# Kernel optimization log

Measured on AMD Instinct MI355X. Metric: run time of the kernel, lower is better.

The kernel has to match this reference:

```python
import jax, jax.numpy as jnp
import numpy as np

THRESH = 0.5
MARGIN = 0.1
SCALE_POS = 2.0
SCALE_NEG = 40.0
EPS = 1e-5


def setup_inputs() -> dict:
    key = jax.random.key(0)
    k1, k2 = jax.random.split(key)
    B, D, C = 8192, 512, 512
    feats = jax.random.normal(k1, (B, D), dtype=jnp.float32)
    labels = jax.random.randint(k2, (B,), 0, C, dtype=jnp.int32)
    return {"feats": feats, "labels": labels}


def reference(feats, labels):
    B = feats.shape[0]
    inv_b = 1.0 / B
    # L2-normalize rows, cosine similarity matrix [B, B]
    f = feats / jnp.linalg.norm(feats, axis=1, keepdims=True)
    sim = f @ f.T

    same = labels[:, None] == labels[None, :]
    # positive pairs: same label AND sim < 1 - eps (excludes self-similarity)
    pos_mask = same & (sim < 1.0 - EPS)
    neg_mask = ~same

    pos_cnt = jnp.sum(pos_mask, axis=1)
    neg_cnt = jnp.sum(neg_mask, axis=1)
    valid1 = (pos_cnt >= 1) & (neg_cnt >= 1)  # row contributes to avg_ap/avg_an

    pos_sum_sim = jnp.sum(jnp.where(pos_mask, sim, 0.0), axis=1)
    neg_sum_sim = jnp.sum(jnp.where(neg_mask, sim, 0.0), axis=1)
    mean_pos = pos_sum_sim / jnp.maximum(pos_cnt, 1)
    mean_neg = neg_sum_sim / jnp.maximum(neg_cnt, 1)

    min_pos = jnp.min(jnp.where(pos_mask, sim, jnp.inf), axis=1)
    max_neg = jnp.max(jnp.where(neg_mask, sim, -jnp.inf), axis=1)

    # hard mining: neg_pair + margin > min(pos), pos_pair - margin < max(neg)
    neg_sel = neg_mask & (sim + MARGIN > min_pos[:, None])
    pos_sel = pos_mask & (sim - MARGIN < max_neg[:, None])
    valid2 = (jnp.sum(pos_sel, axis=1) >= 1) & (jnp.sum(neg_sel, axis=1) >= 1)
    valid = valid1 & valid2

    pos_exp = jnp.sum(jnp.where(pos_sel, jnp.exp(-SCALE_POS * (sim - THRESH)), 0.0), axis=1)
    neg_exp = jnp.sum(jnp.where(neg_sel, jnp.exp(SCALE_NEG * (sim - THRESH)), 0.0), axis=1)
    row_loss = (1.0 / SCALE_POS) * jnp.log1p(pos_exp) + (1.0 / SCALE_NEG) * jnp.log1p(neg_exp)

    loss = jnp.sum(jnp.where(valid, row_loss, 0.0)) * inv_b
    avg_ap = jnp.sum(jnp.where(valid1, mean_pos, 0.0)) * inv_b
    avg_an = jnp.sum(jnp.where(valid1, mean_neg, 0.0)) * inv_b
    return (loss.reshape(-1), avg_ap, avg_an)
```

## Files before the change

kernel.cpp:

```cpp
#include <hip/hip_runtime.h>
#include <math.h>

typedef float floatx4 __attribute__((ext_vector_type(4)));
typedef short short8 __attribute__((ext_vector_type(8)));
typedef unsigned short ushort4v __attribute__((ext_vector_type(4)));
typedef unsigned short ushort8v __attribute__((ext_vector_type(8)));

#define MARGIN_ 0.1f
#define THRESH_ 0.5f

__device__ __forceinline__ unsigned short f2bf(float f){
  unsigned int x = __float_as_uint(f);
  x += 0x7FFFu + ((x >> 16) & 1u);
  return (unsigned short)(x >> 16);
}
__device__ __forceinline__ float bf2f(unsigned short u){
  return __uint_as_float(((unsigned int)u) << 16);
}

__device__ __forceinline__ void gld16(const unsigned short* g, unsigned short* l){
  __builtin_amdgcn_global_load_lds(
      (const __attribute__((address_space(1))) unsigned int*)(g),
      (__attribute__((address_space(3))) unsigned int*)(l), 16, 0, 0);
}

__global__ __launch_bounds__(64) void k_norm(const float* __restrict__ feats,
                                             unsigned short* __restrict__ fbf){
  const int row = blockIdx.x;
  const int l = threadIdx.x;
  const float* rp = feats + (size_t)row * 512;
  float4 v0 = ((const float4*)rp)[2 * l];
  float4 v1 = ((const float4*)rp)[2 * l + 1];
  float ss = v0.x*v0.x + v0.y*v0.y + v0.z*v0.z + v0.w*v0.w
           + v1.x*v1.x + v1.y*v1.y + v1.z*v1.z + v1.w*v1.w;
  #pragma unroll
  for(int m = 1; m < 64; m <<= 1) ss += __shfl_xor(ss, m);
  const float rn = 1.0f / sqrtf(ss);
  short8 pk;
  pk[0] = (short)f2bf(v0.x*rn); pk[1] = (short)f2bf(v0.y*rn);
  pk[2] = (short)f2bf(v0.z*rn); pk[3] = (short)f2bf(v0.w*rn);
  pk[4] = (short)f2bf(v1.x*rn); pk[5] = (short)f2bf(v1.y*rn);
  pk[6] = (short)f2bf(v1.z*rn); pk[7] = (short)f2bf(v1.w*rn);
  ((short8*)(fbf + (size_t)row * 512))[l] = pk;
}

__global__ __launch_bounds__(256) void k_prep(const int* __restrict__ labels,
                                              unsigned short* __restrict__ labp,
                                              int* __restrict__ cnt, int Bn){
  const int i = blockIdx.x * 256 + threadIdx.x;
  if(i < Bn){
    labp[i] = (unsigned short)labels[(i & ~63) + ((i & 3) * 16) + ((i >> 2) & 15)];
    atomicAdd(&cnt[labels[i]], 1);
  }
}

#define TRI_S(y) ((y)*n - (((y)*((y)-1))>>1))
__global__ __launch_bounds__(256) void k_gemm_sym(const unsigned short* __restrict__ fbf,
                                                  unsigned short* __restrict__ simb,
                                                  int Bn, int nTri){
  const int n = Bn >> 7;
  int i = blockIdx.x;
  int j;
  if((nTri & 7) == 0){ const int c = nTri >> 3; j = (i & 7) * c + (i >> 3); }
  else j = i;
  int by = (int)(((float)(2*n + 1) - sqrtf((float)((2*n+1)*(2*n+1) - 8*j))) * 0.5f);
  if(by < 0) by = 0;
  while(TRI_S(by + 1) <= j) by++;
  while(TRI_S(by) > j) by--;
  const int bx = by + (j - TRI_S(by));
  const bool diag = (by == bx);

  __shared__ __align__(16) unsigned short Ald[128 * 32];
  __shared__ __align__(16) unsigned short Bld[128 * 32];

  const int t = threadIdx.x;
  const int lane = t & 63, wave = t >> 6;
  const int wm = wave >> 1, wn = wave & 1;
  const int lc = lane & 15, lk = lane >> 4;
  const int row0 = by * 128, col0 = bx * 128;

  floatx4 acc[4][4];
  #pragma unroll
  for(int a = 0; a < 4; a++)
    #pragma unroll
    for(int b2 = 0; b2 < 4; b2++) acc[a][b2] = (floatx4){0.f, 0.f, 0.f, 0.f};

  const int rsub  = lane >> 2;
  const int slotg = (lane & 3) ^ ((lane >> 3) & 3);
  const unsigned short* gA0 = fbf + (size_t)(row0 + wave*32 + rsub) * 512 + slotg * 8;
  const unsigned short* gB0 = fbf + (size_t)(col0 + wave*32 + rsub) * 512 + slotg * 8;
  unsigned short* lA0 = Ald + wave * 1024;
  unsigned short* lB0 = Bld + wave * 1024;
  const int kswz = lk ^ ((lc >> 1) & 3);

  for(int k0 = 0; k0 < 512; k0 += 32){
    __syncthreads();
    gld16(gA0 + k0,            lA0);
    gld16(gA0 + 16*512 + k0,   lA0 + 512);
    gld16(gB0 + k0,            lB0);
    gld16(gB0 + 16*512 + k0,   lB0 + 512);
    __syncthreads();
    short8 av[4], bv[4];
    #pragma unroll
    for(int mi = 0; mi < 4; mi++) av[mi] = ((const short8*)Ald)[(wm*64 + mi*16 + lc)*4 + kswz];
    #pragma unroll
    for(int ni = 0; ni < 4; ni++) bv[ni] = ((const short8*)Bld)[(wn*64 + ni*16 + lc)*4 + kswz];
    #pragma unroll
    for(int mi = 0; mi < 4; mi++)
      #pragma unroll
      for(int ni = 0; ni < 4; ni++)
        acc[mi][ni] = __builtin_amdgcn_mfma_f32_16x16x32_bf16(av[mi], bv[ni], acc[mi][ni], 0, 0, 0);
  }

  unsigned short b[4][4][4];
  #pragma unroll
  for(int mi = 0; mi < 4; mi++)
    #pragma unroll
    for(int ni = 0; ni < 4; ni++)
      #pragma unroll
      for(int r = 0; r < 4; r++) b[mi][ni][r] = f2bf(acc[mi][ni][r]);

  #pragma unroll
  for(int mi = 0; mi < 4; mi++){
    #pragma unroll
    for(int r = 0; r < 4; r++){
      const int row = row0 + wm*64 + mi*16 + lk*4 + r;
      ushort4v v;
      v[0] = b[mi][0][r]; v[1] = b[mi][1][r]; v[2] = b[mi][2][r]; v[3] = b[mi][3][r];
      *(ushort4v*)(simb + (size_t)row * Bn + col0 + wn*64 + lc*4) = v;
    }
  }

  if(!diag){
    #pragma unroll
    for(int ni = 0; ni < 4; ni++){
      const size_t crow = (size_t)(col0 + wn*64 + ni*16 + lc) * Bn;
      #pragma unroll
      for(int h = 0; h < 2; h++){
        ushort8v v;
        v[0] = b[0][ni][2*h];   v[1] = b[1][ni][2*h];
        v[2] = b[2][ni][2*h];   v[3] = b[3][ni][2*h];
        v[4] = b[0][ni][2*h+1]; v[5] = b[1][ni][2*h+1];
        v[6] = b[2][ni][2*h+1]; v[7] = b[3][ni][2*h+1];
        *(ushort8v*)(simb + crow + row0 + wm*64 + 16*lk + 8*h) = v;
      }
    }
  }
}

template<int NPT>
__global__ __launch_bounds__(256) void k_fused4(const unsigned short* __restrict__ simb,
                                                const int* __restrict__ labels,
                                                const unsigned short* __restrict__ labp,
                                                const int* __restrict__ cnt,
                                                float* __restrict__ rl,
                                                float* __restrict__ apv,
                                                float* __restrict__ anv, int Bn){
  const int t = threadIdx.x, lane = t & 63, wave = t >> 6;
  __shared__ float rq0[4], rq1[4], rq2[4], rq3[4];
  __shared__ int fl[2];

  for(int rr = 0; rr < 4; rr++){
    const int row = blockIdx.x * 4 + rr;
    __syncthreads();
    if(t < 2) fl[t] = 0;
    __syncthreads();

    const unsigned short* srow = simb + (size_t)row * Bn;
    const int labi = labels[row];
    const int a = row & 63;
    const int selfpos = (row & ~63) + ((a & 15) * 4) + (a >> 4);

    ushort8v sv[NPT];
    unsigned int pmask[NPT], nmask[NPT];

    float ps = 0.f, tot = 0.f, mn = INFINITY, mx = -INFINITY;
    #pragma unroll
    for(int c = 0; c < NPT; c++){
      const int idx = c * 256 + t;
      sv[c] = ((const ushort8v*)srow)[idx];
      const ushort8v lb = ((const ushort8v*)labp)[idx];
      const int j0 = idx * 8;
      const unsigned int selfm =
          ((unsigned int)(selfpos - j0) < 8u) ? (1u << (selfpos - j0)) : 0u;
      unsigned int sm = 0;
      #pragma unroll
      for(int e = 0; e < 8; e++) sm |= (((int)lb[e] == labi) ? 1u : 0u) << e;
      const unsigned int pm = sm & ~selfm;
      pmask[c] = pm;
      nmask[c] = (~sm) & 0xFFu;
      #pragma unroll
      for(int e = 0; e < 8; e++){
        const float s = bf2f(sv[c][e]);
        tot += s;
        const bool p = (pm >> e) & 1u;
        const bool nn = (nmask[c] >> e) & 1u;
        ps += p ? s : 0.f;
        mn = p ? fminf(mn, s) : mn;
        mx = nn ? fmaxf(mx, s) : mx;
      }
      if(selfm) tot -= bf2f(sv[c][selfpos - j0]);
    }
    #pragma unroll
    for(int m = 1; m < 64; m <<= 1){
      ps += __shfl_xor(ps, m); tot += __shfl_xor(tot, m);
      mn = fminf(mn, __shfl_xor(mn, m)); mx = fmaxf(mx, __shfl_xor(mx, m));
    }
    if(lane == 0){ rq0[wave] = ps; rq1[wave] = tot; rq2[wave] = mn; rq3[wave] = mx; }
    __syncthreads();
    const float bps    = rq0[0] + rq0[1] + rq0[2] + rq0[3];
    const float btot   = rq1[0] + rq1[1] + rq1[2] + rq1[3];
    const float minpos = fminf(fminf(rq2[0], rq2[1]), fminf(rq2[2], rq2[3]));
    const float maxneg = fmaxf(fmaxf(rq3[0], rq3[1]), fmaxf(rq3[2], rq3[3]));
    __syncthreads();

    float pe = 0.f, ne = 0.f;
    bool pA = false, nA = false;
    #pragma unroll
    for(int c = 0; c < NPT; c++){
      #pragma unroll
      for(int e = 0; e < 8; e++){
        const float s = bf2f(sv[c][e]);
        const bool psel = ((pmask[c] >> e) & 1u) && (s - MARGIN_ < maxneg);
        const bool nsel = ((nmask[c] >> e) & 1u) && (s + MARGIN_ > minpos);
        const float arg = psel ? (THRESH_ - s) * 2.0f : (s - THRESH_) * 40.0f;
        const float ex = __expf(arg);
        pe += psel ? ex : 0.f;
        ne += nsel ? ex : 0.f;
        pA = pA || psel;
        nA = nA || nsel;
      }
    }
    const unsigned long long bp = __ballot((int)pA);
    const unsigned long long bn = __ballot((int)nA);
    #pragma unroll
    for(int m = 1; m < 64; m <<= 1){
      pe += __shfl_xor(pe, m); ne += __shfl_xor(ne, m);
    }
    if(lane == 0){
      rq0[wave] = pe; rq1[wave] = ne;
      if(bp) fl[0] = 1;
      if(bn) fl[1] = 1;
    }
    __syncthreads();
    if(t == 0){
      const float spe = rq0[0] + rq0[1] + rq0[2] + rq0[3];
      const float sne = rq1[0] + rq1[1] + rq1[2] + rq1[3];
      const int c = cnt[labi];
      const float pc = (float)(c - 1);
      const float nc = (float)(Bn - c);
      const bool v1 = (pc >= 1.f) && (nc >= 1.f);
      const bool valid = v1 && (fl[0] != 0) && (fl[1] != 0);
      rl[row]  = valid ? (0.5f * log1pf(spe) + 0.025f * log1pf(sne)) : 0.f;
      apv[row] = v1 ? bps / fmaxf(pc, 1.f) : 0.f;
      anv[row] = v1 ? (btot - bps) / fmaxf(nc, 1.f) : 0.f;
    }
  }
}

__global__ __launch_bounds__(256) void k_fused_gen(const unsigned short* __restrict__ simb,
                                                   const int* __restrict__ labels,
                                                   const unsigned short* __restrict__ labp,
                                                   const int* __restrict__ cnt,
                                                   float* __restrict__ rl,
                                                   float* __restrict__ apv,
                                                   float* __restrict__ anv, int Bn){
  const int row = blockIdx.x;
  const int t = threadIdx.x, lane = t & 63, wave = t >> 6;
  const unsigned short* srow = simb + (size_t)row * Bn;
  const int labi = labels[row];
  const int a = row & 63;
  const int selfpos = (row & ~63) + ((a & 15) * 4) + (a >> 4);
  const int npt = Bn >> 11;

  __shared__ float rq0[4], rq1[4], rq2[4], rq3[4];
  __shared__ int fl[2];
  if(t < 2) fl[t] = 0;

  float ps = 0.f, tot = 0.f, mn = INFINITY, mx = -INFINITY;
  for(int c2 = 0; c2 < npt; c2++){
    const int idx = c2 * 256 + t;
    const ushort8v svv = ((const ushort8v*)srow)[idx];
    const ushort8v lb = ((const ushort8v*)labp)[idx];
    const int j0 = idx * 8;
    #pragma unroll
    for(int e = 0; e < 8; e++){
      const float s = bf2f(svv[e]);
      const bool same = ((int)lb[e] == labi);
      const bool self = ((j0 + e) == selfpos);
      if(!self) tot += s;
      if(same && !self){ ps += s; mn = fminf(mn, s); }
      if(!same) mx = fmaxf(mx, s);
    }
  }
  #pragma unroll
  for(int m = 1; m < 64; m <<= 1){
    ps += __shfl_xor(ps, m); tot += __shfl_xor(tot, m);
    mn = fminf(mn, __shfl_xor(mn, m)); mx = fmaxf(mx, __shfl_xor(mx, m));
  }
  if(lane == 0){ rq0[wave] = ps; rq1[wave] = tot; rq2[wave] = mn; rq3[wave] = mx; }
  __syncthreads();
  const float bps    = rq0[0] + rq0[1] + rq0[2] + rq0[3];
  const float btot   = rq1[0] + rq1[1] + rq1[2] + rq1[3];
  const float minpos = fminf(fminf(rq2[0], rq2[1]), fminf(rq2[2], rq2[3]));
  const float maxneg = fmaxf(fmaxf(rq3[0], rq3[1]), fmaxf(rq3[2], rq3[3]));
  __syncthreads();

  float pe = 0.f, ne = 0.f;
  bool pA = false, nA = false;
  for(int c2 = 0; c2 < npt; c2++){
    const int idx = c2 * 256 + t;
    const ushort8v svv = ((const ushort8v*)srow)[idx];
    const ushort8v lb = ((const ushort8v*)labp)[idx];
    const int j0 = idx * 8;
    #pragma unroll
    for(int e = 0; e < 8; e++){
      const float s = bf2f(svv[e]);
      const bool same = ((int)lb[e] == labi);
      const bool self = ((j0 + e) == selfpos);
      const bool psel = same && !self && (s - MARGIN_ < maxneg);
      const bool nsel = (!same) && (s + MARGIN_ > minpos);
      const float arg = psel ? (THRESH_ - s) * 2.0f : (s - THRESH_) * 40.0f;
      const float ex = __expf(arg);
      pe += psel ? ex : 0.f;
      ne += nsel ? ex : 0.f;
      pA = pA || psel;
      nA = nA || nsel;
    }
  }
  const unsigned long long bp = __ballot((int)pA);
  const unsigned long long bn = __ballot((int)nA);
  #pragma unroll
  for(int m = 1; m < 64; m <<= 1){
    pe += __shfl_xor(pe, m); ne += __shfl_xor(ne, m);
  }
  if(lane == 0){
    rq0[wave] = pe; rq1[wave] = ne;
    if(bp) fl[0] = 1;
    if(bn) fl[1] = 1;
  }
  __syncthreads();
  if(t == 0){
    const float spe = rq0[0] + rq0[1] + rq0[2] + rq0[3];
    const float sne = rq1[0] + rq1[1] + rq1[2] + rq1[3];
    const int c = cnt[labi];
    const float pc = (float)(c - 1);
    const float nc = (float)(Bn - c);
    const bool v1 = (pc >= 1.f) && (nc >= 1.f);
    const bool valid = v1 && (fl[0] != 0) && (fl[1] != 0);
    rl[row]  = valid ? (0.5f * log1pf(spe) + 0.025f * log1pf(sne)) : 0.f;
    apv[row] = v1 ? bps / fmaxf(pc, 1.f) : 0.f;
    anv[row] = v1 ? (btot - bps) / fmaxf(nc, 1.f) : 0.f;
  }
}

__global__ __launch_bounds__(256) void k_sum(const float* __restrict__ rl,
                                             const float* __restrict__ apv,
                                             const float* __restrict__ anv,
                                             float* __restrict__ blk, int Bn){
  const int t = threadIdx.x;
  const int row = blockIdx.x * 256 + t;
  float r = rl[row], a1 = apv[row], a2 = anv[row];
  #pragma unroll
  for(int off = 32; off; off >>= 1){
    r += __shfl_down(r, off); a1 += __shfl_down(a1, off); a2 += __shfl_down(a2, off);
  }
  __shared__ float red[3][4];
  const int lane = t & 63, wave = t >> 6;
  if(lane == 0){ red[0][wave] = r; red[1][wave] = a1; red[2][wave] = a2; }
  __syncthreads();
  if(t == 0){
    blk[blockIdx.x*3 + 0] = red[0][0] + red[0][1] + red[0][2] + red[0][3];
    blk[blockIdx.x*3 + 1] = red[1][0] + red[1][1] + red[1][2] + red[1][3];
    blk[blockIdx.x*3 + 2] = red[2][0] + red[2][1] + red[2][2] + red[2][3];
  }
}

__global__ void k_final(const float* __restrict__ blk, int nblk, float inv_b,
                        float* __restrict__ out){
  if(threadIdx.x == 0 && blockIdx.x == 0){
    float l = 0, a = 0, n = 0;
    for(int i = 0; i < nblk; i++){ l += blk[i*3]; a += blk[i*3 + 1]; n += blk[i*3 + 2]; }
    out[0] = l * inv_b;
    out[1] = a * inv_b;
    out[2] = n * inv_b;
  }
}

__global__ __launch_bounds__(256) void k_pass1(const unsigned short* __restrict__ fbf,
                                               const int* __restrict__ labels,
                                               float* __restrict__ part,
                                               int Bn, int ncb){
  __shared__ __align__(16) unsigned short Ald[128 * 32];
  __shared__ __align__(16) unsigned short Bld[128 * 32];
  __shared__ int Lrow[128], Lcol[128];
  __shared__ float Sps[2][128], Stot[2][128], Smin[2][128], Smax[2][128];

  const int t = threadIdx.x;
  const int lane = t & 63, wave = t >> 6;
  const int wm = wave >> 1, wn = wave & 1;
  const int lc = lane & 15, lk = lane >> 4;
  const int row0 = blockIdx.y * 128, col0 = blockIdx.x * 128;

  if(t < 128){
    Lrow[t] = labels[row0 + t];
    Lcol[t] = labels[col0 + t];
  }

  floatx4 acc[4][4];
  #pragma unroll
  for(int i = 0; i < 4; i++)
    #pragma unroll
    for(int j = 0; j < 4; j++) acc[i][j] = (floatx4){0.f, 0.f, 0.f, 0.f};

  const int rsub  = lane >> 2;
  const int slotg = (lane & 3) ^ ((lane >> 3) & 3);
  const unsigned short* gA0 = fbf + (size_t)(row0 + wave*32 + rsub) * 512 + slotg * 8;
  const unsigned short* gB0 = fbf + (size_t)(col0 + wave*32 + rsub) * 512 + slotg * 8;
  unsigned short* lA0 = Ald + wave * 1024;
  unsigned short* lB0 = Bld + wave * 1024;
  const int kswz = lk ^ ((lc >> 1) & 3);

  for(int k0 = 0; k0 < 512; k0 += 32){
    __syncthreads();
    gld16(gA0 + k0,            lA0);
    gld16(gA0 + 16*512 + k0,   lA0 + 512);
    gld16(gB0 + k0,            lB0);
    gld16(gB0 + 16*512 + k0,   lB0 + 512);
    __syncthreads();
    short8 av[4], bv[4];
    #pragma unroll
    for(int mi = 0; mi < 4; mi++) av[mi] = ((const short8*)Ald)[(wm*64 + mi*16 + lc)*4 + kswz];
    #pragma unroll
    for(int ni = 0; ni < 4; ni++) bv[ni] = ((const short8*)Bld)[(wn*64 + ni*16 + lc)*4 + kswz];
    #pragma unroll
    for(int mi = 0; mi < 4; mi++)
      #pragma unroll
      for(int ni = 0; ni < 4; ni++)
        acc[mi][ni] = __builtin_amdgcn_mfma_f32_16x16x32_bf16(av[mi], bv[ni], acc[mi][ni], 0, 0, 0);
  }

  int labj[4], gj[4];
  #pragma unroll
  for(int ni = 0; ni < 4; ni++){
    const int cl = wn*64 + ni*16 + lc;
    labj[ni] = Lcol[cl]; gj[ni] = col0 + cl;
  }
  #pragma unroll
  for(int mi = 0; mi < 4; mi++){
    #pragma unroll
    for(int r = 0; r < 4; r++){
      const int rowl = wm*64 + mi*16 + lk*4 + r;
      const int labi = Lrow[rowl];
      const int gi = row0 + rowl;
      float ps = 0.f, tot = 0.f, mn = INFINITY, mx = -INFINITY;
      #pragma unroll
      for(int ni = 0; ni < 4; ni++){
        const float s = acc[mi][ni][r];
        const bool same = (labi == labj[ni]);
        const bool self = (gi == gj[ni]);
        if(!self) tot += s;
        if(same && !self){ ps += s; mn = fminf(mn, s); }
        if(!same) mx = fmaxf(mx, s);
      }
      #pragma unroll
      for(int m = 1; m < 16; m <<= 1){
        ps += __shfl_xor(ps, m); tot += __shfl_xor(tot, m);
        mn = fminf(mn, __shfl_xor(mn, m)); mx = fmaxf(mx, __shfl_xor(mx, m));
      }
      if(lc == 0){
        Sps[wn][rowl] = ps; Stot[wn][rowl] = tot;
        Smin[wn][rowl] = mn; Smax[wn][rowl] = mx;
      }
    }
  }
  __syncthreads();
  if(t < 128){
    const size_t stride = (size_t)ncb * Bn;
    const size_t base = (size_t)blockIdx.x * Bn + row0 + t;
    part[0*stride + base] = Sps[0][t] + Sps[1][t];
    part[1*stride + base] = Stot[0][t] + Stot[1][t];
    part[2*stride + base] = fminf(Smin[0][t], Smin[1][t]);
    part[3*stride + base] = fmaxf(Smax[0][t], Smax[1][t]);
  }
}

__global__ __launch_bounds__(256) void k_reduce1(const float* __restrict__ part,
                                                 const int* __restrict__ labels,
                                                 const int* __restrict__ cnt,
                                                 float* __restrict__ st,
                                                 int Bn, int ncb){
  const int row = blockIdx.x * 256 + threadIdx.x;
  if(row >= Bn) return;
  const size_t stride = (size_t)ncb * Bn;
  float ps = 0, tot = 0, mn = INFINITY, mx = -INFINITY;
  for(int cb = 0; cb < ncb; cb++){
    const size_t base = (size_t)cb * Bn + row;
    ps  += part[0*stride + base];
    tot += part[1*stride + base];
    mn = fminf(mn, part[2*stride + base]);
    mx = fmaxf(mx, part[3*stride + base]);
  }
  const int c = cnt[labels[row]];
  const float pc = (float)(c - 1);
  const float nc = (float)(Bn - c);
  st[0*Bn + row] = mn;
  st[1*Bn + row] = mx;
  st[2*Bn + row] = ps / fmaxf(pc, 1.f);
  st[3*Bn + row] = (tot - ps) / fmaxf(nc, 1.f);
  st[4*Bn + row] = (pc >= 1.f && nc >= 1.f) ? 1.f : 0.f;
}

__global__ __launch_bounds__(256) void k_pass2(const unsigned short* __restrict__ fbf,
                                               const int* __restrict__ labels,
                                               const float* __restrict__ st,
                                               float* __restrict__ part,
                                               int Bn, int ncb){
  __shared__ __align__(16) unsigned short Ald[128 * 32];
  __shared__ __align__(16) unsigned short Bld[128 * 32];
  __shared__ int Lrow[128], Lcol[128];
  __shared__ float Minp[128], Maxn[128];
  __shared__ float Spe[2][128], Sne[2][128], Spf[2][128], Snf[2][128];

  const int t = threadIdx.x;
  const int lane = t & 63, wave = t >> 6;
  const int wm = wave >> 1, wn = wave & 1;
  const int lc = lane & 15, lk = lane >> 4;
  const int row0 = blockIdx.y * 128, col0 = blockIdx.x * 128;

  if(t < 128){
    Lrow[t] = labels[row0 + t];
    Lcol[t] = labels[col0 + t];
    Minp[t] = st[0*Bn + row0 + t];
    Maxn[t] = st[1*Bn + row0 + t];
  }

  floatx4 acc[4][4];
  #pragma unroll
  for(int i = 0; i < 4; i++)
    #pragma unroll
    for(int j = 0; j < 4; j++) acc[i][j] = (floatx4){0.f, 0.f, 0.f, 0.f};

  const int rsub  = lane >> 2;
  const int slotg = (lane & 3) ^ ((lane >> 3) & 3);
  const unsigned short* gA0 = fbf + (size_t)(row0 + wave*32 + rsub) * 512 + slotg * 8;
  const unsigned short* gB0 = fbf + (size_t)(col0 + wave*32 + rsub) * 512 + slotg * 8;
  unsigned short* lA0 = Ald + wave * 1024;
  unsigned short* lB0 = Bld + wave * 1024;
  const int kswz = lk ^ ((lc >> 1) & 3);

  for(int k0 = 0; k0 < 512; k0 += 32){
    __syncthreads();
    gld16(gA0 + k0,            lA0);
    gld16(gA0 + 16*512 + k0,   lA0 + 512);
    gld16(gB0 + k0,            lB0);
    gld16(gB0 + 16*512 + k0,   lB0 + 512);
    __syncthreads();
    short8 av[4], bv[4];
    #pragma unroll
    for(int mi = 0; mi < 4; mi++) av[mi] = ((const short8*)Ald)[(wm*64 + mi*16 + lc)*4 + kswz];
    #pragma unroll
    for(int ni = 0; ni < 4; ni++) bv[ni] = ((const short8*)Bld)[(wn*64 + ni*16 + lc)*4 + kswz];
    #pragma unroll
    for(int mi = 0; mi < 4; mi++)
      #pragma unroll
      for(int ni = 0; ni < 4; ni++)
        acc[mi][ni] = __builtin_amdgcn_mfma_f32_16x16x32_bf16(av[mi], bv[ni], acc[mi][ni], 0, 0, 0);
  }

  int labj[4], gj[4];
  #pragma unroll
  for(int ni = 0; ni < 4; ni++){
    const int cl = wn*64 + ni*16 + lc;
    labj[ni] = Lcol[cl]; gj[ni] = col0 + cl;
  }
  #pragma unroll
  for(int mi = 0; mi < 4; mi++){
    #pragma unroll
    for(int r = 0; r < 4; r++){
      const int rowl = wm*64 + mi*16 + lk*4 + r;
      const int labi = Lrow[rowl];
      const int gi = row0 + rowl;
      const float mp  = Minp[rowl];
      const float mxn = Maxn[rowl];
      float pe = 0.f, ne = 0.f;
      bool pa = false, na = false;
      #pragma unroll
      for(int ni = 0; ni < 4; ni++){
        const float s = acc[mi][ni][r];
        const bool same = (labi == labj[ni]);
        const bool self = (gi == gj[ni]);
        if(same && !self && (s - MARGIN_ < mxn)){
          pe += __expf(-2.0f * (s - THRESH_)); pa = true;
        }
        if(!same && (s + MARGIN_ > mp)){
          ne += __expf(40.0f * (s - THRESH_)); na = true;
        }
      }
      const unsigned long long bp  = __ballot((int)pa);
      const unsigned long long bn2 = __ballot((int)na);
      #pragma unroll
      for(int m = 1; m < 16; m <<= 1){
        pe += __shfl_xor(pe, m); ne += __shfl_xor(ne, m);
      }
      if(lc == 0){
        Spe[wn][rowl] = pe; Sne[wn][rowl] = ne;
        Spf[wn][rowl] = ((bp  >> (lk*16)) & 0xFFFFull) ? 1.f : 0.f;
        Snf[wn][rowl] = ((bn2 >> (lk*16)) & 0xFFFFull) ? 1.f : 0.f;
      }
    }
  }
  __syncthreads();
  if(t < 128){
    const size_t stride = (size_t)ncb * Bn;
    const size_t base = (size_t)blockIdx.x * Bn + row0 + t;
    part[0*stride + base] = Spe[0][t] + Spe[1][t];
    part[1*stride + base] = Sne[0][t] + Sne[1][t];
    part[2*stride + base] = fmaxf(Spf[0][t], Spf[1][t]);
    part[3*stride + base] = fmaxf(Snf[0][t], Snf[1][t]);
  }
}

__global__ __launch_bounds__(256) void k_reduce2f(const float* __restrict__ part,
                                                  const float* __restrict__ st,
                                                  float* __restrict__ rowloss,
                                                  float* __restrict__ apv,
                                                  float* __restrict__ anv,
                                                  int Bn, int ncb){
  const int row = blockIdx.x * 256 + threadIdx.x;
  if(row >= Bn) return;
  const size_t stride = (size_t)ncb * Bn;
  float pe = 0, ne = 0, pf = 0, nf = 0;
  for(int cb = 0; cb < ncb; cb++){
    const size_t base = (size_t)cb * Bn + row;
    pe += part[0*stride + base]; ne += part[1*stride + base];
    pf = fmaxf(pf, part[2*stride + base]); nf = fmaxf(nf, part[3*stride + base]);
  }
  const float v1 = st[4*Bn + row];
  const bool valid = (v1 > 0.5f) && (pf > 0.5f) && (nf > 0.5f);
  rowloss[row] = valid ? (0.5f * log1pf(pe) + 0.025f * log1pf(ne)) : 0.f;
  apv[row] = (v1 > 0.5f) ? st[2*Bn + row] : 0.f;
  anv[row] = (v1 > 0.5f) ? st[3*Bn + row] : 0.f;
}

extern "C" void kernel_launch(void* const* d_in, const int* in_sizes, int n_in,
                              void* d_out, int out_size, void* d_ws, size_t ws_size,
                              hipStream_t stream){
  const float* feats = (const float*)d_in[0];
  const int* labels = (const int*)d_in[1];
  float* out = (float*)d_out;
  const int Bn  = in_sizes[1];
  const int ncb = Bn / 128;
  const int nTri = ncb * (ncb + 1) / 2;

  char* ws = (char*)d_ws;
  size_t off = 0;
  unsigned short* fbf = (unsigned short*)(ws + off); off += (size_t)Bn * 512 * 2;
  float* part = (float*)(ws + off); off += (size_t)4 * ncb * Bn * 4;
  float* st   = (float*)(ws + off); off += (size_t)5 * Bn * 4;
  int*   cnt  = (int*)(ws + off);   off += 4096;
  unsigned short* labp = (unsigned short*)(ws + off); off += (size_t)Bn * 2;
  off = (off + 255) & ~(size_t)255;
  float* rl   = (float*)(ws + off); off += (size_t)Bn * 4;
  float* apv  = (float*)(ws + off); off += (size_t)Bn * 4;
  float* anv  = (float*)(ws + off); off += (size_t)Bn * 4;
  float* blk  = (float*)(ws + off); off += 4096;
  off = (off + 255) & ~(size_t)255;
  unsigned short* simb = (unsigned short*)(ws + off);
  const size_t need = off + (size_t)Bn * Bn * 2;
  const bool mat = (ws_size >= need);

  hipMemsetAsync(cnt, 0, 512 * sizeof(int), stream);
  k_norm<<<Bn, 64, 0, stream>>>(feats, fbf);
  k_prep<<<(Bn + 255) / 256, 256, 0, stream>>>(labels, labp, cnt, Bn);
  if(mat){
    k_gemm_sym<<<nTri, 256, 0, stream>>>(fbf, simb, Bn, nTri);
    if(Bn == 8192){
      k_fused4<4><<<Bn / 4, 256, 0, stream>>>(simb, labels, labp, cnt, rl, apv, anv, Bn);
    } else {
      k_fused_gen<<<Bn, 256, 0, stream>>>(simb, labels, labp, cnt, rl, apv, anv, Bn);
    }
  } else {
    dim3 g(ncb, Bn / 128);
    k_pass1<<<g, 256, 0, stream>>>(fbf, labels, part, Bn, ncb);
    k_reduce1<<<Bn / 256, 256, 0, stream>>>(part, labels, cnt, st, Bn, ncb);
    k_pass2<<<g, 256, 0, stream>>>(fbf, labels, st, part, Bn, ncb);
    k_reduce2f<<<Bn / 256, 256, 0, stream>>>(part, st, rl, apv, anv, Bn, ncb);
  }
  k_sum<<<Bn / 256, 256, 0, stream>>>(rl, apv, anv, blk, Bn);
  k_final<<<1, 64, 0, stream>>>(blk, Bn / 256, 1.0f / (float)Bn, out);
}
```

Before: 161.6 us.

## Use one row per block in fused pass, replace ballot flags with analytic validity

The fused row-reduction kernel now assigns one row per block (grid Bn) instead of looping four rows per block, which removes the per-row barriers and the flag-reset syncs. The any-selected flags are replaced by a closed-form check: a positive is selected iff minpos - margin < maxneg, and a negative iff maxneg + margin > minpos. This drops the ballots and shared flags. The exponent becomes a single exp2f of an fma with log2e-folded constants, and bf16 unpacking works on 32-bit words with shifts and masks. More blocks means more scheduling overhead but more memory-level parallelism. The validity rewrite relies on the min/max equivalence also holding for NaN and infinity edge cases.

```diff
diff --git a/kernel.cpp b/kernel.cpp
--- a/kernel.cpp
+++ b/kernel.cpp
@@ -5,9 +5,11 @@
 typedef short short8 __attribute__((ext_vector_type(8)));
 typedef unsigned short ushort4v __attribute__((ext_vector_type(4)));
 typedef unsigned short ushort8v __attribute__((ext_vector_type(8)));
+typedef unsigned int uint4v __attribute__((ext_vector_type(4)));
 
 #define MARGIN_ 0.1f
 #define THRESH_ 0.5f
+#define LOG2E_ 1.44269504088896f
 
 __device__ __forceinline__ unsigned short f2bf(float f){
   unsigned int x = __float_as_uint(f);
@@ -149,112 +151,116 @@
 }
 
 template<int NPT>
-__global__ __launch_bounds__(256) void k_fused4(const unsigned short* __restrict__ simb,
-                                                const int* __restrict__ labels,
-                                                const unsigned short* __restrict__ labp,
-                                                const int* __restrict__ cnt,
-                                                float* __restrict__ rl,
-                                                float* __restrict__ apv,
-                                                float* __restrict__ anv, int Bn){
+__global__ __launch_bounds__(256) void k_fused(const unsigned short* __restrict__ simb,
+                                               const int* __restrict__ labels,
+                                               const unsigned short* __restrict__ labp,
+                                               const int* __restrict__ cnt,
+                                               float* __restrict__ rl,
+                                               float* __restrict__ apv,
+                                               float* __restrict__ anv, int Bn){
+  const int row = blockIdx.x;
   const int t = threadIdx.x, lane = t & 63, wave = t >> 6;
+  const unsigned short* srow = simb + (size_t)row * Bn;
+  const int labi = labels[row];
+  const int a = row & 63;
+  const int selfpos = (row & ~63) + ((a & 15) * 4) + (a >> 4);
+
   __shared__ float rq0[4], rq1[4], rq2[4], rq3[4];
-  __shared__ int fl[2];
-
-  for(int rr = 0; rr < 4; rr++){
-    const int row = blockIdx.x * 4 + rr;
-    __syncthreads();
-    if(t < 2) fl[t] = 0;
-    __syncthreads();
-
-    const unsigned short* srow = simb + (size_t)row * Bn;
-    const int labi = labels[row];
-    const int a = row & 63;
-    const int selfpos = (row & ~63) + ((a & 15) * 4) + (a >> 4);
-
-    ushort8v sv[NPT];
-    unsigned int pmask[NPT], nmask[NPT];
-
-    float ps = 0.f, tot = 0.f, mn = INFINITY, mx = -INFINITY;
-    #pragma unroll
-    for(int c = 0; c < NPT; c++){
-      const int idx = c * 256 + t;
-      sv[c] = ((const ushort8v*)srow)[idx];
-      const ushort8v lb = ((const ushort8v*)labp)[idx];
-      const int j0 = idx * 8;
-      const unsigned int selfm =
-          ((unsigned int)(selfpos - j0) < 8u) ? (1u << (selfpos - j0)) : 0u;
-      unsigned int sm = 0;
-      #pragma unroll
-      for(int e = 0; e < 8; e++) sm |= (((int)lb[e] == labi) ? 1u : 0u) << e;
-      const unsigned int pm = sm & ~selfm;
-      pmask[c] = pm;
-      nmask[c] = (~sm) & 0xFFu;
-      #pragma unroll
-      for(int e = 0; e < 8; e++){
-        const float s = bf2f(sv[c][e]);
-        tot += s;
-        const bool p = (pm >> e) & 1u;
-        const bool nn = (nmask[c] >> e) & 1u;
-        ps += p ? s : 0.f;
-        mn = p ? fminf(mn, s) : mn;
-        mx = nn ? fmaxf(mx, s) : mx;
-      }
-      if(selfm) tot -= bf2f(sv[c][selfpos - j0]);
-    }
-    #pragma unroll
-    for(int m = 1; m < 64; m <<= 1){
-      ps += __shfl_xor(ps, m); tot += __shfl_xor(tot, m);
-      mn = fminf(mn, __shfl_xor(mn, m)); mx = fmaxf(mx, __shfl_xor(mx, m));
-    }
-    if(lane == 0){ rq0[wave] = ps; rq1[wave] = tot; rq2[wave] = mn; rq3[wave] = mx; }
-    __syncthreads();
-    const float bps    = rq0[0] + rq0[1] + rq0[2] + rq0[3];
-    const float btot   = rq1[0] + rq1[1] + rq1[2] + rq1[3];
-    const float minpos = fminf(fminf(rq2[0], rq2[1]), fminf(rq2[2], rq2[3]));
-    const float maxneg = fmaxf(fmaxf(rq3[0], rq3[1]), fmaxf(rq3[2], rq3[3]));
-    __syncthreads();
-
-    float pe = 0.f, ne = 0.f;
-    bool pA = false, nA = false;
-    #pragma unroll
-    for(int c = 0; c < NPT; c++){
-      #pragma unroll
-      for(int e = 0; e < 8; e++){
-        const float s = bf2f(sv[c][e]);
-        const bool psel = ((pmask[c] >> e) & 1u) && (s - MARGIN_ < maxneg);
-        const bool nsel = ((nmask[c] >> e) & 1u) && (s + MARGIN_ > minpos);
-        const float arg = psel ? (THRESH_ - s) * 2.0f : (s - THRESH_) * 40.0f;
-        const float ex = __expf(arg);
+
+  uint4v sv[NPT];
+  unsigned int pmask[NPT], nmask[NPT];
+
+  float ps = 0.f, tot = 0.f, mn = INFINITY, mx = -INFINITY;
+  #pragma unroll
+  for(int c = 0; c < NPT; c++){
+    const int idx = c * 256 + t;
+    sv[c] = ((const uint4v*)srow)[idx];
+    const uint4v lb = ((const uint4v*)labp)[idx];
+    const int j0 = idx * 8;
+    const int so = selfpos - j0;
+    const unsigned int selfm = ((unsigned int)so < 8u) ? (1u << so) : 0u;
+    unsigned int sm = 0;
+    #pragma unroll
+    for(int k = 0; k < 4; k++){
+      const unsigned int lw = lb[k];
+      sm |= (((int)(lw & 0xFFFFu) == labi) ? 1u : 0u) << (2*k);
+      sm |= (((int)(lw >> 16)     == labi) ? 1u : 0u) << (2*k + 1);
+    }
+    const unsigned int pm = sm & ~selfm;
+    pmask[c] = pm;
+    nmask[c] = (~sm) & 0xFFu;
+    #pragma unroll
+    for(int k = 0; k < 4; k++){
+      const unsigned int w = sv[c][k];
+      const float slo = __uint_as_float(w << 16);
+      const float shi = __uint_as_float(w & 0xFFFF0000u);
+      tot += slo + shi;
+      const bool plo = (pm >> (2*k)) & 1u,  phi = (pm >> (2*k+1)) & 1u;
+      const bool nlo = (nmask[c] >> (2*k)) & 1u, nhi = (nmask[c] >> (2*k+1)) & 1u;
+      ps += plo ? slo : 0.f;  ps += phi ? shi : 0.f;
+      mn = plo ? fminf(mn, slo) : mn;  mn = phi ? fminf(mn, shi) : mn;
+      mx = nlo ? fmaxf(mx, slo) : mx;  mx = nhi ? fmaxf(mx, shi) : mx;
+    }
+    if(selfm){
+      const unsigned int w = sv[c][so >> 1];
+      tot -= (so & 1) ? __uint_as_float(w & 0xFFFF0000u) : __uint_as_float(w << 16);
+    }
+  }
+  #pragma unroll
+  for(int m = 1; m < 64; m <<= 1){
+    ps += __shfl_xor(ps, m); tot += __shfl_xor(tot, m);
+    mn = fminf(mn, __shfl_xor(mn, m)); mx = fmaxf(mx, __shfl_xor(mx, m));
+  }
+  if(lane == 0){ rq0[wave] = ps; rq1[wave] = tot; rq2[wave] = mn; rq3[wave] = mx; }
+  __syncthreads();
+  const float bps    = rq0[0] + rq0[1] + rq0[2] + rq0[3];
+  const float btot   = rq1[0] + rq1[1] + rq1[2] + rq1[3];
+  const float minpos = fminf(fminf(rq2[0], rq2[1]), fminf(rq2[2], rq2[3]));
+  const float maxneg = fmaxf(fmaxf(rq3[0], rq3[1]), fmaxf(rq3[2], rq3[3]));
+
+  const float KP1 = -2.0f * LOG2E_, KP0 = 1.0f * LOG2E_;
+  const float KN1 = 40.0f * LOG2E_, KN0 = -20.0f * LOG2E_;
+  float pe = 0.f, ne = 0.f;
+  #pragma unroll
+  for(int c = 0; c < NPT; c++){
+    const unsigned int pm = pmask[c], nm = nmask[c];
+    #pragma unroll
+    for(int k = 0; k < 4; k++){
+      const unsigned int w = sv[c][k];
+      #pragma unroll
+      for(int h = 0; h < 2; h++){
+        const float s = h ? __uint_as_float(w & 0xFFFF0000u)
+                          : __uint_as_float(w << 16);
+        const int e = 2*k + h;
+        const bool isp = (pm >> e) & 1u;
+        const bool isn = (nm >> e) & 1u;
+        const float ex = exp2f(fmaf(s, isp ? KP1 : KN1, isp ? KP0 : KN0));
+        const bool psel = isp && (s - MARGIN_ < maxneg);
+        const bool nsel = isn && (s + MARGIN_ > minpos);
         pe += psel ? ex : 0.f;
         ne += nsel ? ex : 0.f;
-        pA = pA || psel;
-        nA = nA || nsel;
-      }
-    }
-    const unsigned long long bp = __ballot((int)pA);
-    const unsigned long long bn = __ballot((int)nA);
-    #pragma unroll
-    for(int m = 1; m < 64; m <<= 1){
-      pe += __shfl_xor(pe, m); ne += __shfl_xor(ne, m);
-    }
-    if(lane == 0){
-      rq0[wave] = pe; rq1[wave] = ne;
-      if(bp) fl[0] = 1;
-      if(bn) fl[1] = 1;
-    }
-    __syncthreads();
-    if(t == 0){
-      const float spe = rq0[0] + rq0[1] + rq0[2] + rq0[3];
-      const float sne = rq1[0] + rq1[1] + rq1[2] + rq1[3];
-      const int c = cnt[labi];
-      const float pc = (float)(c - 1);
-      const float nc = (float)(Bn - c);
-      const bool v1 = (pc >= 1.f) && (nc >= 1.f);
-      const bool valid = v1 && (fl[0] != 0) && (fl[1] != 0);
-      rl[row]  = valid ? (0.5f * log1pf(spe) + 0.025f * log1pf(sne)) : 0.f;
-      apv[row] = v1 ? bps / fmaxf(pc, 1.f) : 0.f;
-      anv[row] = v1 ? (btot - bps) / fmaxf(nc, 1.f) : 0.f;
-    }
+      }
+    }
+  }
+  #pragma unroll
+  for(int m = 1; m < 64; m <<= 1){
+    pe += __shfl_xor(pe, m); ne += __shfl_xor(ne, m);
+  }
+  if(lane == 0){ rq0[wave] = pe; rq1[wave] = ne; }
+  __syncthreads();
+  if(t == 0){
+    const float spe = rq0[0] + rq0[1] + rq0[2] + rq0[3];
+    const float sne = rq1[0] + rq1[1] + rq1[2] + rq1[3];
+    const int c = cnt[labi];
+    const float pc = (float)(c - 1);
+    const float nc = (float)(Bn - c);
+    const bool v1 = (pc >= 1.f) && (nc >= 1.f);
+    const bool pf = (minpos - MARGIN_ < maxneg);
+    const bool nf = (maxneg + MARGIN_ > minpos);
+    const bool valid = v1 && pf && nf;
+    rl[row]  = valid ? (0.5f * log1pf(spe) + 0.025f * log1pf(sne)) : 0.f;
+    apv[row] = v1 ? bps / fmaxf(pc, 1.f) : 0.f;
+    anv[row] = v1 ? (btot - bps) / fmaxf(nc, 1.f) : 0.f;
   }
 }
 
@@ -274,8 +280,6 @@
   const int npt = Bn >> 11;
 
   __shared__ float rq0[4], rq1[4], rq2[4], rq3[4];
-  __shared__ int fl[2];
-  if(t < 2) fl[t] = 0;
 
   float ps = 0.f, tot = 0.f, mn = INFINITY, mx = -INFINITY;
   for(int c2 = 0; c2 < npt; c2++){
@@ -304,10 +308,8 @@
   const float btot   = rq1[0] + rq1[1] + rq1[2] + rq1[3];
   const float minpos = fminf(fminf(rq2[0], rq2[1]), fminf(rq2[2], rq2[3]));
   const float maxneg = fmaxf(fmaxf(rq3[0], rq3[1]), fmaxf(rq3[2], rq3[3]));
-  __syncthreads();
 
   float pe = 0.f, ne = 0.f;
-  bool pA = false, nA = false;
   for(int c2 = 0; c2 < npt; c2++){
     const int idx = c2 * 256 + t;
     const ushort8v svv = ((const ushort8v*)srow)[idx];
@@ -320,25 +322,17 @@
       const bool self = ((j0 + e) == selfpos);
       const bool psel = same && !self && (s - MARGIN_ < maxneg);
       const bool nsel = (!same) && (s + MARGIN_ > minpos);
-      const float arg = psel ? (THRESH_ - s) * 2.0f : (s - THRESH_) * 40.0f;
-      const float ex = __expf(arg);
+      const float ex = exp2f(fmaf(s, psel ? (-2.0f*LOG2E_) : (40.0f*LOG2E_),
+                                     psel ? LOG2E_ : (-20.0f*LOG2E_)));
       pe += psel ? ex : 0.f;
       ne += nsel ? ex : 0.f;
-      pA = pA || psel;
-      nA = nA || nsel;
-    }
-  }
-  const unsigned long long bp = __ballot((int)pA);
-  const unsigned long long bn = __ballot((int)nA);
+    }
+  }
   #pragma unroll
   for(int m = 1; m < 64; m <<= 1){
     pe += __shfl_xor(pe, m); ne += __shfl_xor(ne, m);
   }
-  if(lane == 0){
-    rq0[wave] = pe; rq1[wave] = ne;
-    if(bp) fl[0] = 1;
-    if(bn) fl[1] = 1;
-  }
+  if(lane == 0){ rq0[wave] = pe; rq1[wave] = ne; }
   __syncthreads();
   if(t == 0){
     const float spe = rq0[0] + rq0[1] + rq0[2] + rq0[3];
@@ -347,7 +341,9 @@
     const float pc = (float)(c - 1);
     const float nc = (float)(Bn - c);
     const bool v1 = (pc >= 1.f) && (nc >= 1.f);
-    const bool valid = v1 && (fl[0] != 0) && (fl[1] != 0);
+    const bool pf = (minpos - MARGIN_ < maxneg);
+    const bool nf = (maxneg + MARGIN_ > minpos);
+    const bool valid = v1 && pf && nf;
     rl[row]  = valid ? (0.5f * log1pf(spe) + 0.025f * log1pf(sne)) : 0.f;
     apv[row] = v1 ? bps / fmaxf(pc, 1.f) : 0.f;
     anv[row] = v1 ? (btot - bps) / fmaxf(nc, 1.f) : 0.f;
@@ -670,13 +666,13 @@
   const size_t need = off + (size_t)Bn * Bn * 2;
   const bool mat = (ws_size >= need);
 
-  hipMemsetAsync(cnt, 0, 512 * sizeof(int), stream);
+  (void)hipMemsetAsync(cnt, 0, 512 * sizeof(int), stream);
   k_norm<<<Bn, 64, 0, stream>>>(feats, fbf);
   k_prep<<<(Bn + 255) / 256, 256, 0, stream>>>(labels, labp, cnt, Bn);
   if(mat){
     k_gemm_sym<<<nTri, 256, 0, stream>>>(fbf, simb, Bn, nTri);
     if(Bn == 8192){
-      k_fused4<4><<<Bn / 4, 256, 0, stream>>>(simb, labels, labp, cnt, rl, apv, anv, Bn);
+      k_fused<4><<<Bn, 256, 0, stream>>>(simb, labels, labp, cnt, rl, apv, anv, Bn);
     } else {
       k_fused_gen<<<Bn, 256, 0, stream>>>(simb, labels, labp, cnt, rl, apv, anv, Bn);
     }
```

Result: faster. 153.5 us (-5.0%).
